# Optimization experiments

Measured on AMD Instinct MI355X. Metric: run time of the kernel, lower is better.

The kernel has to match this reference:

```python
import jax, jax.numpy as jnp
import numpy as np

S = 128          # voxel grid resolution per axis
NPB = 50000      # active voxels per batch element
B = 2            # batch size
C_IN = 64
C_OUT = 64
K = 3            # kernel size

# kernel offsets in [-1,0,1]^3, shape [27, 3]
_OFFS = np.stack(np.meshgrid(np.arange(-1, 2), np.arange(-1, 2), np.arange(-1, 2), indexing='ij'), axis=-1).reshape(-1, 3)


def setup_inputs() -> dict:
    rng = np.random.default_rng(0)
    coords_list = []
    for b in range(B):
        lin = rng.choice(S * S * S, size=NPB, replace=False)  # unique voxels
        x = lin // (S * S)
        y = (lin // S) % S
        z = lin % S
        coords_list.append(np.stack([np.full(NPB, b), x, y, z], axis=1))
    coords = jnp.asarray(np.concatenate(coords_list, axis=0), dtype=jnp.int32)  # [N,4]

    key = jax.random.key(0)
    k1, k2, k3 = jax.random.split(key, 3)
    feats = jax.random.normal(k1, (B * NPB, C_IN), dtype=jnp.float32)
    fan1 = C_IN * K ** 3
    fan2 = C_OUT * K ** 3
    W1 = jax.random.normal(k2, (K ** 3, C_IN, C_OUT), dtype=jnp.float32) / np.sqrt(fan1)
    W2 = jax.random.normal(k3, (K ** 3, C_OUT, C_OUT), dtype=jnp.float32) / np.sqrt(fan2)
    return {"feats": feats, "coords": coords, "W1": W1, "W2": W2}


def _encode(coords):
    # linear key: ((b*S + x)*S + y)*S + z ; fits in int32 for S=128, B small
    b, x, y, z = coords[:, 0], coords[:, 1], coords[:, 2], coords[:, 3]
    return ((b * S + x) * S + y) * S + z


def _sparse_conv(feats, coords, W):
    """Stride-1 sparse (submanifold-style) 3D conv: output coords == input coords.
    feats [N,Cin], coords [N,4], W [27,Cin,Cout] -> [N,Cout]."""
    N = feats.shape[0]
    keys = _encode(coords)
    order = jnp.argsort(keys)
    skeys = keys[order]
    offs = jnp.asarray(_OFFS, dtype=jnp.int32)  # [27,3]

    def gather_one(d):
        qxyz = coords[:, 1:4] + d[None, :]
        valid = jnp.all((qxyz >= 0) & (qxyz < S), axis=1)
        qkey = keys + (d[0] * S * S + d[1] * S + d[2])
        idx = jnp.clip(jnp.searchsorted(skeys, qkey), 0, N - 1)
        found = valid & (skeys[idx] == qkey)
        return jnp.where(found[:, None], feats[order[idx]], 0.0)  # [N,Cin]

    gathered = jax.vmap(gather_one)(offs)  # [27, N, Cin]
    return jnp.einsum('onc,ocd->nd', gathered, W)


def reference(feats, coords, W1, W2):
    h = _sparse_conv(feats, coords, W1)
    out = _sparse_conv(h, coords, W2)
    return out
```

## Files before the change

### kernel.cpp

```cpp
#include <hip/hip_runtime.h>
#include <stdint.h>

#define SGRID 128
#define CAP 4096

typedef _Float16 f16;
typedef f16 f16x8 __attribute__((ext_vector_type(8)));
typedef float f32x4 __attribute__((ext_vector_type(4)));

static __device__ __forceinline__ f32x4 mfma16(uint4 a, uint4 b, f32x4 c) {
    union { uint4 u; f16x8 v; } ua, ub;
    ua.u = a; ub.u = b;
    return __builtin_amdgcn_mfma_f32_16x16x32_f16(ua.v, ub.v, c, 0, 0, 0);
}

static __device__ __forceinline__ void split8(const float* v, uint4& hu, uint4& lu) {
    union { f16 h[8]; uint4 u; } hv, lv;
    #pragma unroll
    for (int j = 0; j < 8; ++j) {
        f16 h = (f16)v[j];
        hv.h[j] = h;
        lv.h[j] = (f16)(v[j] - (float)h);
    }
    hu = hv.u; lu = lv.u;
}

__global__ void clear_meta(uint4* __restrict__ bitmap4, int nwords4, int* __restrict__ cnt) {
    int i = blockIdx.x * 256 + threadIdx.x;
    if (i < nwords4) bitmap4[i] = (uint4){0, 0, 0, 0};
    if (blockIdx.x == 0 && threadIdx.x < 26) cnt[threadIdx.x * 16] = 0;
}

__global__ void scatter_table(const int* __restrict__ coords, int* __restrict__ table,
                              unsigned* __restrict__ bitmap, int n) {
    int i = blockIdx.x * blockDim.x + threadIdx.x;
    if (i >= n) return;
    int4 c = ((const int4*)coords)[i];
    int key = ((c.x * SGRID + c.y) * SGRID + c.z) * SGRID + c.w;
    table[key] = i;
    atomicOr(&bitmap[key >> 5], 1u << (key & 31));
}

__global__ void __launch_bounds__(256) build_pairs(
    const int* __restrict__ coords, const int* __restrict__ table,
    const unsigned* __restrict__ bitmap,
    int* __restrict__ pin, int* __restrict__ pout,
    int* __restrict__ cnt, int N)
{
    __shared__ unsigned long long sbal[26][4];
    __shared__ int sbase[26];

    const int tid  = threadIdx.x;
    const int lane = tid & 63;
    const int wave = tid >> 6;
    const int n    = blockIdx.x * 256 + tid;
    const bool valid = n < N;

    int4 c = {0, 0, 0, 0};
    if (valid) c = ((const int4*)coords)[n];
    const int key = ((c.x * SGRID + c.y) * SGRID + c.z) * SGRID + c.w;

    int nb[26];
    #pragma unroll
    for (int slot = 0; slot < 26; ++slot) {
        int o = slot < 13 ? slot : slot + 1;
        int dx = o / 9 - 1, dy = (o / 3) % 3 - 1, dz = o % 3 - 1;
        int qx = c.y + dx, qy = c.z + dy, qz = c.w + dz;
        nb[slot] = -1;
        if (valid && (unsigned)qx < SGRID && (unsigned)qy < SGRID && (unsigned)qz < SGRID) {
            int qkey = key + (dx * SGRID * SGRID + dy * SGRID + dz);
            if ((bitmap[qkey >> 5] >> (qkey & 31)) & 1u)
                nb[slot] = table[qkey];
        }
    }

    #pragma unroll
    for (int slot = 0; slot < 26; ++slot) {
        unsigned long long bal = __ballot(nb[slot] >= 0);
        if (lane == 0) sbal[slot][wave] = bal;
    }
    __syncthreads();

    if (tid < 26) {
        int tot = (int)__popcll(sbal[tid][0]) + (int)__popcll(sbal[tid][1])
                + (int)__popcll(sbal[tid][2]) + (int)__popcll(sbal[tid][3]);
        int base = 0;
        if (tot) base = atomicAdd(&cnt[tid * 16], tot);
        sbase[tid] = base;
    }
    __syncthreads();

    #pragma unroll
    for (int slot = 0; slot < 26; ++slot) {
        if (nb[slot] >= 0) {
            int rank = (int)__popcll(sbal[slot][wave] & ((1ull << lane) - 1ull));
            #pragma unroll
            for (int w = 0; w < 4; ++w)
                if (w < wave) rank += (int)__popcll(sbal[slot][w]);
            int pos = sbase[slot] + rank;
            if (pos < CAP) {
                pin[slot * CAP + pos]  = nb[slot];
                pout[slot * CAP + pos] = n;
            }
        }
    }
}

__global__ void prep_w(const float* __restrict__ W1, const float* __restrict__ W2,
                       f16* __restrict__ Wp1, f16* __restrict__ Wp2) {
    int idx = blockIdx.x * blockDim.x + threadIdx.x;
    const int half = 27 * 4 * 2 * 64;
    if (idx >= 2 * half) return;
    const float* W = (idx < half) ? W1 : W2;
    f16* Wp = (idx < half) ? Wp1 : Wp2;
    int id = (idx < half) ? idx : idx - half;
    int lane = id & 63;
    int ks = (id >> 6) & 1;
    int ct = (id >> 7) & 3;
    int o  = id >> 9;
    int co  = ct * 16 + (lane & 15);
    int ci0 = ks * 32 + (lane >> 4) * 8;
    union { f16 h[8]; uint4 u; } hv;
    #pragma unroll
    for (int j = 0; j < 8; ++j)
        hv.h[j] = (f16)W[((size_t)o * 64 + ci0 + j) * 64 + co];
    ((uint4*)Wp)[id] = hv.u;
}

__global__ void __launch_bounds__(256) conv_center(
    const float* __restrict__ A, const f16* __restrict__ Wp,
    float* __restrict__ O, int N)
{
    int gw = (blockIdx.x * 256 + threadIdx.x) >> 6;
    int ngroups = (N + 31) >> 5;
    if (gw >= ngroups) return;
    const int lane = threadIdx.x & 63, r = lane & 15, lq = lane >> 4;
    const int p0 = gw * 32;

    const uint4* wb = (const uint4*)Wp + 13 * 512 + lane;
    uint4 b[2][4];
    #pragma unroll
    for (int ct = 0; ct < 4; ++ct)
        #pragma unroll
        for (int ks = 0; ks < 2; ++ks)
            b[ks][ct] = wb[(ct * 2 + ks) * 64];

    uint4 ah[2][2], al[2][2];
    #pragma unroll
    for (int rt = 0; rt < 2; ++rt) {
        int row = p0 + rt * 16 + r;
        #pragma unroll
        for (int ks = 0; ks < 2; ++ks) {
            float v[8];
            if (row < N) {
                float4 v0 = *(const float4*)(A + (size_t)row * 64 + ks * 32 + lq * 8);
                float4 v1 = *(const float4*)(A + (size_t)row * 64 + ks * 32 + lq * 8 + 4);
                v[0]=v0.x; v[1]=v0.y; v[2]=v0.z; v[3]=v0.w;
                v[4]=v1.x; v[5]=v1.y; v[6]=v1.z; v[7]=v1.w;
            } else {
                #pragma unroll
                for (int j = 0; j < 8; ++j) v[j] = 0.f;
            }
            split8(v, ah[rt][ks], al[rt][ks]);
        }
    }

    f32x4 acc[2][4];
    #pragma unroll
    for (int i = 0; i < 2; ++i)
        #pragma unroll
        for (int j = 0; j < 4; ++j) acc[i][j] = (f32x4){0.f, 0.f, 0.f, 0.f};

    #pragma unroll
    for (int ks = 0; ks < 2; ++ks)
        #pragma unroll
        for (int rt = 0; rt < 2; ++rt)
            #pragma unroll
            for (int ct = 0; ct < 4; ++ct) {
                acc[rt][ct] = mfma16(ah[rt][ks], b[ks][ct], acc[rt][ct]);
                acc[rt][ct] = mfma16(al[rt][ks], b[ks][ct], acc[rt][ct]);
            }

    #pragma unroll
    for (int rt = 0; rt < 2; ++rt)
        #pragma unroll
        for (int j = 0; j < 4; ++j) {
            int row = p0 + rt * 16 + lq * 4 + j;
            if (row < N) {
                #pragma unroll
                for (int ct = 0; ct < 4; ++ct)
                    O[(size_t)row * 64 + ct * 16 + r] = acc[rt][ct][j];
            }
        }
}

__global__ void __launch_bounds__(256) conv_sparse(
    const float* __restrict__ A, const f16* __restrict__ Wp,
    const int* __restrict__ pin, const int* __restrict__ pout,
    const int* __restrict__ cnt, float* __restrict__ O)
{
    int gw = (blockIdx.x * 256 + threadIdx.x) >> 6;
    int slot = gw >> 7;
    int chunk = gw & 127;
    if (slot >= 26) return;
    int cn = cnt[slot * 16]; if (cn > CAP) cn = CAP;
    int i0 = chunk * 32;
    if (i0 >= cn) return;
    int o = slot < 13 ? slot : slot + 1;
    const int lane = threadIdx.x & 63, r = lane & 15, lq = lane >> 4;

    const uint4* wb = (const uint4*)Wp + (size_t)o * 512 + lane;
    uint4 b[2][4];
    #pragma unroll
    for (int ct = 0; ct < 4; ++ct)
        #pragma unroll
        for (int ks = 0; ks < 2; ++ks)
            b[ks][ct] = wb[(ct * 2 + ks) * 64];

    uint4 ah[2][2], al[2][2];
    #pragma unroll
    for (int rt = 0; rt < 2; ++rt) {
        int p = i0 + rt * 16 + r;
        int in = (p < cn) ? pin[slot * CAP + p] : -1;
        #pragma unroll
        for (int ks = 0; ks < 2; ++ks) {
            float v[8];
            if (in >= 0) {
                float4 v0 = *(const float4*)(A + (size_t)in * 64 + ks * 32 + lq * 8);
                float4 v1 = *(const float4*)(A + (size_t)in * 64 + ks * 32 + lq * 8 + 4);
                v[0]=v0.x; v[1]=v0.y; v[2]=v0.z; v[3]=v0.w;
                v[4]=v1.x; v[5]=v1.y; v[6]=v1.z; v[7]=v1.w;
            } else {
                #pragma unroll
                for (int j = 0; j < 8; ++j) v[j] = 0.f;
            }
            split8(v, ah[rt][ks], al[rt][ks]);
        }
    }

    f32x4 acc[2][4];
    #pragma unroll
    for (int i = 0; i < 2; ++i)
        #pragma unroll
        for (int j = 0; j < 4; ++j) acc[i][j] = (f32x4){0.f, 0.f, 0.f, 0.f};

    #pragma unroll
    for (int ks = 0; ks < 2; ++ks)
        #pragma unroll
        for (int rt = 0; rt < 2; ++rt)
            #pragma unroll
            for (int ct = 0; ct < 4; ++ct) {
                acc[rt][ct] = mfma16(ah[rt][ks], b[ks][ct], acc[rt][ct]);
                acc[rt][ct] = mfma16(al[rt][ks], b[ks][ct], acc[rt][ct]);
            }

    #pragma unroll
    for (int rt = 0; rt < 2; ++rt)
        #pragma unroll
        for (int j = 0; j < 4; ++j) {
            int p = i0 + rt * 16 + lq * 4 + j;
            if (p < cn) {
                int oidx = pout[slot * CAP + p];
                #pragma unroll
                for (int ct = 0; ct < 4; ++ct)
                    atomicAdd(&O[(size_t)oidx * 64 + ct * 16 + r], acc[rt][ct][j]);
            }
        }
}

extern "C" void kernel_launch(void* const* d_in, const int* in_sizes, int n_in,
                              void* d_out, int out_size, void* d_ws, size_t ws_size,
                              hipStream_t stream) {
    const float* feats  = (const float*)d_in[0];
    const int*   coords = (const int*)d_in[1];
    const float* W1     = (const float*)d_in[2];
    const float* W2     = (const float*)d_in[3];
    float* out = (float*)d_out;

    const int N = in_sizes[0] / 64;
    const size_t nvox = 2ull * SGRID * SGRID * SGRID;

    char* p = (char*)d_ws;
    int*      table  = (int*)p;      p += nvox * 4;
    unsigned* bitmap = (unsigned*)p; p += (nvox / 32) * 4;
    int*      cnt    = (int*)p;      p += 26 * 16 * 4;
    int*      pin    = (int*)p;      p += 26ull * CAP * 4;
    int*      pout   = (int*)p;      p += 26ull * CAP * 4;
    float*    H      = (float*)p;    p += (size_t)N * 64 * 4;
    f16*      Wp1    = (f16*)p;      p += 27ull * 4096 * 2;
    f16*      Wp2    = (f16*)p;      p += 27ull * 4096 * 2;

    const int bm4 = (int)(nvox / 32 / 4);
    clear_meta<<<(bm4 + 255) / 256, 256, 0, stream>>>((uint4*)bitmap, bm4, cnt);
    scatter_table<<<(N + 255) / 256, 256, 0, stream>>>(coords, table, bitmap, N);
    prep_w<<<(2 * 27 * 4 * 2 * 64 + 255) / 256, 256, 0, stream>>>(W1, W2, Wp1, Wp2);
    build_pairs<<<(N + 255) / 256, 256, 0, stream>>>(coords, table, bitmap, pin, pout, cnt, N);

    const int ngroups = (N + 31) / 32;
    const int cblocks = (ngroups + 3) / 4;
    const int sblocks = 26 * 128 / 4;

    conv_center<<<cblocks, 256, 0, stream>>>(feats, Wp1, H, N);
    conv_sparse<<<sblocks, 256, 0, stream>>>(feats, Wp1, pin, pout, cnt, H);
    conv_center<<<cblocks, 256, 0, stream>>>(H, Wp2, out, N);
    conv_sparse<<<sblocks, 256, 0, stream>>>(H, Wp2, pin, pout, cnt, out);
}
```

Baseline: 111.6 us.

## Merge independent setup kernels and split sparse conv waves finer

Fuses scatter_table with weight prep, and the pair-building pass with the first center convolution, into shared launches that branch on block index. This removes two launches and lets independent work run side by side. The sparse conv now gives each wave 16 pairs and half the output channels instead of 32 pairs and all 64 channels. That raises the wave count and lowers per-wave register use for better occupancy, at the cost of redundant index and feature loads.

```diff
diff --git a/kernel.cpp b/kernel.cpp
--- a/kernel.cpp
+++ b/kernel.cpp
@@ -25,116 +25,11 @@
     hu = hv.u; lu = lv.u;
 }
 
-__global__ void clear_meta(uint4* __restrict__ bitmap4, int nwords4, int* __restrict__ cnt) {
-    int i = blockIdx.x * 256 + threadIdx.x;
-    if (i < nwords4) bitmap4[i] = (uint4){0, 0, 0, 0};
-    if (blockIdx.x == 0 && threadIdx.x < 26) cnt[threadIdx.x * 16] = 0;
-}
-
-__global__ void scatter_table(const int* __restrict__ coords, int* __restrict__ table,
-                              unsigned* __restrict__ bitmap, int n) {
-    int i = blockIdx.x * blockDim.x + threadIdx.x;
-    if (i >= n) return;
-    int4 c = ((const int4*)coords)[i];
-    int key = ((c.x * SGRID + c.y) * SGRID + c.z) * SGRID + c.w;
-    table[key] = i;
-    atomicOr(&bitmap[key >> 5], 1u << (key & 31));
-}
-
-__global__ void __launch_bounds__(256) build_pairs(
-    const int* __restrict__ coords, const int* __restrict__ table,
-    const unsigned* __restrict__ bitmap,
-    int* __restrict__ pin, int* __restrict__ pout,
-    int* __restrict__ cnt, int N)
-{
-    __shared__ unsigned long long sbal[26][4];
-    __shared__ int sbase[26];
-
-    const int tid  = threadIdx.x;
-    const int lane = tid & 63;
-    const int wave = tid >> 6;
-    const int n    = blockIdx.x * 256 + tid;
-    const bool valid = n < N;
-
-    int4 c = {0, 0, 0, 0};
-    if (valid) c = ((const int4*)coords)[n];
-    const int key = ((c.x * SGRID + c.y) * SGRID + c.z) * SGRID + c.w;
-
-    int nb[26];
-    #pragma unroll
-    for (int slot = 0; slot < 26; ++slot) {
-        int o = slot < 13 ? slot : slot + 1;
-        int dx = o / 9 - 1, dy = (o / 3) % 3 - 1, dz = o % 3 - 1;
-        int qx = c.y + dx, qy = c.z + dy, qz = c.w + dz;
-        nb[slot] = -1;
-        if (valid && (unsigned)qx < SGRID && (unsigned)qy < SGRID && (unsigned)qz < SGRID) {
-            int qkey = key + (dx * SGRID * SGRID + dy * SGRID + dz);
-            if ((bitmap[qkey >> 5] >> (qkey & 31)) & 1u)
-                nb[slot] = table[qkey];
-        }
-    }
-
-    #pragma unroll
-    for (int slot = 0; slot < 26; ++slot) {
-        unsigned long long bal = __ballot(nb[slot] >= 0);
-        if (lane == 0) sbal[slot][wave] = bal;
-    }
-    __syncthreads();
-
-    if (tid < 26) {
-        int tot = (int)__popcll(sbal[tid][0]) + (int)__popcll(sbal[tid][1])
-                + (int)__popcll(sbal[tid][2]) + (int)__popcll(sbal[tid][3]);
-        int base = 0;
-        if (tot) base = atomicAdd(&cnt[tid * 16], tot);
-        sbase[tid] = base;
-    }
-    __syncthreads();
-
-    #pragma unroll
-    for (int slot = 0; slot < 26; ++slot) {
-        if (nb[slot] >= 0) {
-            int rank = (int)__popcll(sbal[slot][wave] & ((1ull << lane) - 1ull));
-            #pragma unroll
-            for (int w = 0; w < 4; ++w)
-                if (w < wave) rank += (int)__popcll(sbal[slot][w]);
-            int pos = sbase[slot] + rank;
-            if (pos < CAP) {
-                pin[slot * CAP + pos]  = nb[slot];
-                pout[slot * CAP + pos] = n;
-            }
-        }
-    }
-}
-
-__global__ void prep_w(const float* __restrict__ W1, const float* __restrict__ W2,
-                       f16* __restrict__ Wp1, f16* __restrict__ Wp2) {
-    int idx = blockIdx.x * blockDim.x + threadIdx.x;
-    const int half = 27 * 4 * 2 * 64;
-    if (idx >= 2 * half) return;
-    const float* W = (idx < half) ? W1 : W2;
-    f16* Wp = (idx < half) ? Wp1 : Wp2;
-    int id = (idx < half) ? idx : idx - half;
-    int lane = id & 63;
-    int ks = (id >> 6) & 1;
-    int ct = (id >> 7) & 3;
-    int o  = id >> 9;
-    int co  = ct * 16 + (lane & 15);
-    int ci0 = ks * 32 + (lane >> 4) * 8;
-    union { f16 h[8]; uint4 u; } hv;
-    #pragma unroll
-    for (int j = 0; j < 8; ++j)
-        hv.h[j] = (f16)W[((size_t)o * 64 + ci0 + j) * 64 + co];
-    ((uint4*)Wp)[id] = hv.u;
-}
-
-__global__ void __launch_bounds__(256) conv_center(
+static __device__ __forceinline__ void center_body(
     const float* __restrict__ A, const f16* __restrict__ Wp,
-    float* __restrict__ O, int N)
-{
-    int gw = (blockIdx.x * 256 + threadIdx.x) >> 6;
-    int ngroups = (N + 31) >> 5;
-    if (gw >= ngroups) return;
-    const int lane = threadIdx.x & 63, r = lane & 15, lq = lane >> 4;
+    float* __restrict__ O, int N, int gw, int lane)
+{
+    const int r = lane & 15, lq = lane >> 4;
     const int p0 = gw * 32;
 
     const uint4* wb = (const uint4*)Wp + 13 * 512 + lane;
@@ -194,78 +89,193 @@
         }
 }
 
+__global__ void clear_meta(uint4* __restrict__ bitmap4, int nwords4, int* __restrict__ cnt) {
+    int i = blockIdx.x * 256 + threadIdx.x;
+    if (i < nwords4) bitmap4[i] = (uint4){0, 0, 0, 0};
+    if (blockIdx.x == 0 && threadIdx.x < 26) cnt[threadIdx.x * 16] = 0;
+}
+
+__global__ void __launch_bounds__(256) scatter_prep(
+    const int* __restrict__ coords, int* __restrict__ table,
+    unsigned* __restrict__ bitmap, int N, int scatB,
+    const float* __restrict__ W1, const float* __restrict__ W2,
+    f16* __restrict__ Wp1, f16* __restrict__ Wp2)
+{
+    const int tid = threadIdx.x;
+    if (blockIdx.x < scatB) {
+        int i = blockIdx.x * 256 + tid;
+        if (i < N) {
+            int4 c = ((const int4*)coords)[i];
+            int key = ((c.x * SGRID + c.y) * SGRID + c.z) * SGRID + c.w;
+            table[key] = i;
+            atomicOr(&bitmap[key >> 5], 1u << (key & 31));
+        }
+        return;
+    }
+    int idx = (blockIdx.x - scatB) * 256 + tid;
+    const int half = 27 * 512;
+    const float* W = (idx < half) ? W1 : W2;
+    f16* Wp = (idx < half) ? Wp1 : Wp2;
+    int id = (idx < half) ? idx : idx - half;
+    int lane = id & 63;
+    int ks = (id >> 6) & 1;
+    int ct = (id >> 7) & 3;
+    int o  = id >> 9;
+    int co  = ct * 16 + (lane & 15);
+    int ci0 = ks * 32 + (lane >> 4) * 8;
+    union { f16 h[8]; uint4 u; } hv;
+    #pragma unroll
+    for (int j = 0; j < 8; ++j)
+        hv.h[j] = (f16)W[((size_t)o * 64 + ci0 + j) * 64 + co];
+    ((uint4*)Wp)[id] = hv.u;
+}
+
+__global__ void __launch_bounds__(256) build_center(
+    const int* __restrict__ coords, const int* __restrict__ table,
+    const unsigned* __restrict__ bitmap,
+    int* __restrict__ pin, int* __restrict__ pout, int* __restrict__ cnt,
+    int N, int buildB,
+    const float* __restrict__ F, const f16* __restrict__ Wp, float* __restrict__ H)
+{
+    __shared__ unsigned long long sbal[26][4];
+    __shared__ int sbase[26];
+    const int tid = threadIdx.x;
+
+    if (blockIdx.x >= buildB) {
+        int gw = ((blockIdx.x - buildB) * 256 + tid) >> 6;
+        if (gw < (N + 31) >> 5)
+            center_body(F, Wp, H, N, gw, tid & 63);
+        return;
+    }
+
+    const int lane = tid & 63;
+    const int wave = tid >> 6;
+    const int n    = blockIdx.x * 256 + tid;
+    const bool valid = n < N;
+
+    int4 c = {0, 0, 0, 0};
+    if (valid) c = ((const int4*)coords)[n];
+    const int key = ((c.x * SGRID + c.y) * SGRID + c.z) * SGRID + c.w;
+
+    int nb[26];
+    #pragma unroll
+    for (int slot = 0; slot < 26; ++slot) {
+        int o = slot < 13 ? slot : slot + 1;
+        int dx = o / 9 - 1, dy = (o / 3) % 3 - 1, dz = o % 3 - 1;
+        int qx = c.y + dx, qy = c.z + dy, qz = c.w + dz;
+        nb[slot] = -1;
+        if (valid && (unsigned)qx < SGRID && (unsigned)qy < SGRID && (unsigned)qz < SGRID) {
+            int qkey = key + (dx * SGRID * SGRID + dy * SGRID + dz);
+            if ((bitmap[qkey >> 5] >> (qkey & 31)) & 1u)
+                nb[slot] = table[qkey];
+        }
+    }
+
+    #pragma unroll
+    for (int slot = 0; slot < 26; ++slot) {
+        unsigned long long bal = __ballot(nb[slot] >= 0);
+        if (lane == 0) sbal[slot][wave] = bal;
+    }
+    __syncthreads();
+
+    if (tid < 26) {
+        int tot = (int)__popcll(sbal[tid][0]) + (int)__popcll(sbal[tid][1])
+                + (int)__popcll(sbal[tid][2]) + (int)__popcll(sbal[tid][3]);
+        int base = 0;
+        if (tot) base = atomicAdd(&cnt[tid * 16], tot);
+        sbase[tid] = base;
+    }
+    __syncthreads();
+
+    #pragma unroll
+    for (int slot = 0; slot < 26; ++slot) {
+        if (nb[slot] >= 0) {
+            int rank = (int)__popcll(sbal[slot][wave] & ((1ull << lane) - 1ull));
+            #pragma unroll
+            for (int w = 0; w < 4; ++w)
+                if (w < wave) rank += (int)__popcll(sbal[slot][w]);
+            int pos = sbase[slot] + rank;
+            if (pos < CAP) {
+                pin[slot * CAP + pos]  = nb[slot];
+                pout[slot * CAP + pos] = n;
+            }
+        }
+    }
+}
+
+__global__ void __launch_bounds__(256) conv_center(
+    const float* __restrict__ A, const f16* __restrict__ Wp,
+    float* __restrict__ O, int N)
+{
+    int gw = (blockIdx.x * 256 + threadIdx.x) >> 6;
+    if (gw < (N + 31) >> 5)
+        center_body(A, Wp, O, N, gw, threadIdx.x & 63);
+}
+
 __global__ void __launch_bounds__(256) conv_sparse(
     const float* __restrict__ A, const f16* __restrict__ Wp,
     const int* __restrict__ pin, const int* __restrict__ pout,
     const int* __restrict__ cnt, float* __restrict__ O)
 {
-    int gw = (blockIdx.x * 256 + threadIdx.x) >> 6;
-    int slot = gw >> 7;
-    int chunk = gw & 127;
-    if (slot >= 26) return;
+    int w = (blockIdx.x * 256 + threadIdx.x) >> 6;
+    if (w >= 26 * 512) return;
+    int slot  = w >> 9;
+    int rem   = w & 511;
+    int chunk = rem >> 1;
+    int ch    = rem & 1;
     int cn = cnt[slot * 16]; if (cn > CAP) cn = CAP;
-    int i0 = chunk * 32;
+    int i0 = chunk * 16;
     if (i0 >= cn) return;
     int o = slot < 13 ? slot : slot + 1;
     const int lane = threadIdx.x & 63, r = lane & 15, lq = lane >> 4;
 
     const uint4* wb = (const uint4*)Wp + (size_t)o * 512 + lane;
-    uint4 b[2][4];
-    #pragma unroll
-    for (int ct = 0; ct < 4; ++ct)
+    uint4 b[2][2];
+    #pragma unroll
+    for (int ct = 0; ct < 2; ++ct)
         #pragma unroll
         for (int ks = 0; ks < 2; ++ks)
-            b[ks][ct] = wb[(ct * 2 + ks) * 64];
-
-    uint4 ah[2][2], al[2][2];
-    #pragma unroll
-    for (int rt = 0; rt < 2; ++rt) {
-        int p = i0 + rt * 16 + r;
-        int in = (p < cn) ? pin[slot * CAP + p] : -1;
-        #pragma unroll
-        for (int ks = 0; ks < 2; ++ks) {
-            float v[8];
-            if (in >= 0) {
-                float4 v0 = *(const float4*)(A + (size_t)in * 64 + ks * 32 + lq * 8);
-                float4 v1 = *(const float4*)(A + (size_t)in * 64 + ks * 32 + lq * 8 + 4);
-                v[0]=v0.x; v[1]=v0.y; v[2]=v0.z; v[3]=v0.w;
-                v[4]=v1.x; v[5]=v1.y; v[6]=v1.z; v[7]=v1.w;
-            } else {
-                #pragma unroll
-                for (int j = 0; j < 8; ++j) v[j] = 0.f;
-            }
-            split8(v, ah[rt][ks], al[rt][ks]);
-        }
-    }
-
-    f32x4 acc[2][4];
-    #pragma unroll
-    for (int i = 0; i < 2; ++i)
-        #pragma unroll
-        for (int j = 0; j < 4; ++j) acc[i][j] = (f32x4){0.f, 0.f, 0.f, 0.f};
-
+            b[ct][ks] = wb[((ch * 2 + ct) * 2 + ks) * 64];
+
+    int p = i0 + r;
+    int in = (p < cn) ? pin[slot * CAP + p] : -1;
+    uint4 ah[2], al[2];
+    #pragma unroll
+    for (int ks = 0; ks < 2; ++ks) {
+        float v[8];
+        if (in >= 0) {
+            float4 v0 = *(const float4*)(A + (size_t)in * 64 + ks * 32 + lq * 8);
+            float4 v1 = *(const float4*)(A + (size_t)in * 64 + ks * 32 + lq * 8 + 4);
+            v[0]=v0.x; v[1]=v0.y; v[2]=v0.z; v[3]=v0.w;
+            v[4]=v1.x; v[5]=v1.y; v[6]=v1.z; v[7]=v1.w;
+        } else {
+            #pragma unroll
+            for (int j = 0; j < 8; ++j) v[j] = 0.f;
+        }
+        split8(v, ah[ks], al[ks]);
+    }
+
+    f32x4 acc[2];
+    acc[0] = (f32x4){0.f, 0.f, 0.f, 0.f};
+    acc[1] = (f32x4){0.f, 0.f, 0.f, 0.f};
     #pragma unroll
     for (int ks = 0; ks < 2; ++ks)
         #pragma unroll
-        for (int rt = 0; rt < 2; ++rt)
+        for (int ct = 0; ct < 2; ++ct) {
+            acc[ct] = mfma16(ah[ks], b[ct][ks], acc[ct]);
+            acc[ct] = mfma16(al[ks], b[ct][ks], acc[ct]);
+        }
+
+    #pragma unroll
+    for (int j = 0; j < 4; ++j) {
+        int pr = i0 + lq * 4 + j;
+        if (pr < cn) {
+            int oidx = pout[slot * CAP + pr];
             #pragma unroll
-            for (int ct = 0; ct < 4; ++ct) {
-                acc[rt][ct] = mfma16(ah[rt][ks], b[ks][ct], acc[rt][ct]);
-                acc[rt][ct] = mfma16(al[rt][ks], b[ks][ct], acc[rt][ct]);
-            }
-
-    #pragma unroll
-    for (int rt = 0; rt < 2; ++rt)
-        #pragma unroll
-        for (int j = 0; j < 4; ++j) {
-            int p = i0 + rt * 16 + lq * 4 + j;
-            if (p < cn) {
-                int oidx = pout[slot * CAP + p];
-                #pragma unroll
-                for (int ct = 0; ct < 4; ++ct)
-                    atomicAdd(&O[(size_t)oidx * 64 + ct * 16 + r], acc[rt][ct][j]);
-            }
-        }
+            for (int ct = 0; ct < 2; ++ct)
+                atomicAdd(&O[(size_t)oidx * 64 + (ch * 2 + ct) * 16 + r], acc[ct][j]);
+        }
+    }
 }
 
 extern "C" void kernel_launch(void* const* d_in, const int* in_sizes, int n_in,
@@ -290,18 +300,20 @@
     f16*      Wp1    = (f16*)p;      p += 27ull * 4096 * 2;
     f16*      Wp2    = (f16*)p;      p += 27ull * 4096 * 2;
 
-    const int bm4 = (int)(nvox / 32 / 4);
+    const int bm4     = (int)(nvox / 32 / 4);
+    const int scatB   = (N + 255) / 256;
+    const int buildB  = scatB;
+    const int ngroups = (N + 31) / 32;
+    const int centerB = (ngroups + 3) / 4;
+    const int sparseB = 26 * 512 / 4;
+
     clear_meta<<<(bm4 + 255) / 256, 256, 0, stream>>>((uint4*)bitmap, bm4, cnt);
-    scatter_table<<<(N + 255) / 256, 256, 0, stream>>>(coords, table, bitmap, N);
-    prep_w<<<(2 * 27 * 4 * 2 * 64 + 255) / 256, 256, 0, stream>>>(W1, W2, Wp1, Wp2);
-    build_pairs<<<(N + 255) / 256, 256, 0, stream>>>(coords, table, bitmap, pin, pout, cnt, N);
-
-    const int ngroups = (N + 31) / 32;
-    const int cblocks = (ngroups + 3) / 4;
-    const int sblocks = 26 * 128 / 4;
-
-    conv_center<<<cblocks, 256, 0, stream>>>(feats, Wp1, H, N);
-    conv_sparse<<<sblocks, 256, 0, stream>>>(feats, Wp1, pin, pout, cnt, H);
-    conv_center<<<cblocks, 256, 0, stream>>>(H, Wp2, out, N);
-    conv_sparse<<<sblocks, 256, 0, stream>>>(H, Wp2, pin, pout, cnt, out);
-}
+    scatter_prep<<<scatB + 108, 256, 0, stream>>>(coords, table, bitmap, N, scatB,
+                                                  W1, W2, Wp1, Wp2);
+    build_center<<<buildB + centerB, 256, 0, stream>>>(coords, table, bitmap,
+                                                       pin, pout, cnt, N, buildB,
+                                                       feats, Wp1, H);
+    conv_sparse<<<sparseB, 256, 0, stream>>>(feats, Wp1, pin, pout, cnt, H);
+    conv_center<<<centerB, 256, 0, stream>>>(H, Wp2, out, N);
+    conv_sparse<<<sparseB, 256, 0, stream>>>(H, Wp2, pin, pout, cnt, out);
+}
```

Measured after the change: 95.77 us. 1.16x faster.
